# Kernel tuning notes

Measured on AMD Instinct MI355X. Metric: run time of the kernel, lower is better.

## Reference

```python
import jax, jax.numpy as jnp
import numpy as np

EPS = 1e-08   # clip eps from __init__
M = 0.2       # angular margin
B, D, C = 512, 512, 100000


def setup_inputs() -> dict:
    key = jax.random.key(0)
    k1, k2, k3 = jax.random.split(key, 3)
    x = jax.random.normal(k1, (B, D), dtype=jnp.float32)
    weight = jax.random.normal(k2, (C, D), dtype=jnp.float32)
    y = jax.random.randint(k3, (B,), 0, C, dtype=jnp.int64)
    rescale = jnp.ones((1,), dtype=jnp.float32)
    return {"x": x, "y": y, "weight": weight, "rescale": rescale}


def _l2norm(v, axis=-1, eps=1e-12):
    # matches F.normalize(p=2): v / max(||v||, eps)
    n = jnp.sqrt(jnp.sum(v * v, axis=axis, keepdims=True))
    return v / jnp.maximum(n, eps)


def reference(x, y, weight, rescale):
    # cos similarities: [B, C]
    fc = jnp.clip(_l2norm(x) @ _l2norm(weight).T, -1.0 + EPS, 1.0 - EPS)
    fc_w_margin = jnp.cos(jnp.arccos(fc) + M)
    # inject margin only at the target class (one-hot where-select)
    is_target = jax.nn.one_hot(y, C, dtype=jnp.bool_)
    logit = jnp.where(is_target, fc_w_margin, fc)
    # faithful to original: softmax, then CrossEntropyLoss on the probs
    res = jax.nn.softmax(rescale * logit, axis=-1)
    logp = jax.nn.log_softmax(res, axis=-1)
    nll = -jnp.take_along_axis(logp, y[:, None], axis=1)[:, 0]
    return jnp.mean(nll)
```

## Files before the change

kernel.cpp:

```cpp
#include <hip/hip_runtime.h>
#include <math.h>

#define BB 512
#define DD 512
#define CC 100000
#define CCPAD 100096
#define MARGIN 0.2f
#define CLIP_EPS 1e-8f
#define NCOLT 782

typedef float f32x4  __attribute__((ext_vector_type(4)));
typedef long  lx2    __attribute__((ext_vector_type(2)));

#define XN8_BYTES   262144u
#define P_BYTES     1601536u
#define PBASE       XN8_BYTES
#define AUX_OFF     (PBASE + 3u * P_BYTES)

__device__ inline unsigned f2e4m3(float a) {
    unsigned u = __builtin_bit_cast(unsigned, a);
    unsigned s = (u >> 24) & 0x80u;
    float ab = fabsf(a);
    unsigned code;
    if (ab >= 0.015625f) {
        unsigned r = (u & 0x7FFFFFFFu) + 0x7FFFFu + ((u >> 20) & 1u);
        int e = (int)(r >> 23) - 127;
        unsigned m = (r >> 20) & 7u;
        code = (unsigned)((e + 7) << 3) | m;
    } else {
        code = (unsigned)rintf(ab * 512.0f);
    }
    return s | code;
}

__device__ inline int soff8(int row, int b) {
    return row * 64 + ((((b >> 4) ^ ((row >> 1) & 3)) << 4)) + (b & 15);
}


__global__ __launch_bounds__(256) void k_prep(const float* __restrict__ w,
                                              const float* __restrict__ x,
                                              unsigned char* __restrict__ WN8,
                                              unsigned char* __restrict__ XN8,
                                              float* __restrict__ out) {
    int wv = threadIdx.x >> 6, lane = threadIdx.x & 63;
    int r = blockIdx.x * 4 + wv;
    const float* src;
    unsigned char* dst;
    bool zero = false;
    if (r < CCPAD) {
        zero = (r >= CC);
        src = w + (size_t)(zero ? 0 : r) * DD;
        dst = WN8 + (size_t)r * DD;
    } else {
        int xr = r - CCPAD;
        src = x + (size_t)xr * DD;
        dst = XN8 + (size_t)xr * DD;
    }
    int o  = lane * 8;
    int K0 = (o & ~63) + ((o >> 3) & 1) * 32 + ((o >> 4) & 3) * 8;
    float4 a = *(const float4*)(src + K0);
    float4 b = *(const float4*)(src + K0 + 4);
    if (zero) { a = make_float4(0.f,0.f,0.f,0.f); b = a; }
    float ss = a.x*a.x + a.y*a.y + a.z*a.z + a.w*a.w
             + b.x*b.x + b.y*b.y + b.z*b.z + b.w*b.w;
    for (int m = 1; m < 64; m <<= 1) ss += __shfl_xor(ss, m, 64);
    float inv = 1.0f / fmaxf(sqrtf(ss), 1e-12f);
    unsigned lo = f2e4m3(a.x*inv) | (f2e4m3(a.y*inv) << 8) | (f2e4m3(a.z*inv) << 16) | (f2e4m3(a.w*inv) << 24);
    unsigned hi = f2e4m3(b.x*inv) | (f2e4m3(b.y*inv) << 8) | (f2e4m3(b.z*inv) << 16) | (f2e4m3(b.w*inv) << 24);
    *(uint2*)(dst + o) = make_uint2(lo, hi);
    if (blockIdx.x == 0 && threadIdx.x == 0) out[0] = 0.0f;
}

__global__ __launch_bounds__(256) void k_gemm8(const unsigned char* __restrict__ WN8,
                                               const unsigned char* __restrict__ XN8,
                                               const float* __restrict__ rescale_p,
                                               float* __restrict__ ZP,
                                               float* __restrict__ S2P,
                                               float* __restrict__ S3P) {
    __shared__ __align__(16) unsigned char Wt[3][128 * 64];
    __shared__ __align__(16) unsigned char Xs[3][128 * 64];
    __shared__ float st[2][2][64][3];

    int h = blockIdx.x;
    int logical = (h & 7) * 391 + (h >> 3);
    int ct = logical >> 2;
    int bt = logical & 3;

    int tid = threadIdx.x;
    int lane = tid & 63, wid = tid >> 6;
    int wr = wid >> 1, wc = wid & 1;
    float rescale = rescale_p[0];

    int rl0 = wid * 16 + (lane >> 2);
    int j0  = lane & 3;
    const unsigned char* wbase = WN8 + (size_t)(ct * 128) * DD;
    const unsigned char* xbase = XN8 + (size_t)(bt * 128) * DD;

    auto STAGE = [&](int b, int kt) {
#pragma unroll
        for (int i = 0; i < 2; ++i) {
            int rl = i * 64 + rl0;
            int jsrc = j0 ^ ((rl >> 1) & 3);
            const unsigned char* ws_ = wbase + (size_t)rl * DD + kt * 64 + jsrc * 16;
            const unsigned char* xs_ = xbase + (size_t)rl * DD + kt * 64 + jsrc * 16;
            unsigned char* wd = &Wt[b][(i * 256 + wid * 64) * 16];
            unsigned char* xd = &Xs[b][(i * 256 + wid * 64) * 16];
            __builtin_amdgcn_global_load_lds(
                (const __attribute__((address_space(1))) void*)ws_,
                (__attribute__((address_space(3))) void*)wd, 16, 0, 0);
            __builtin_amdgcn_global_load_lds(
                (const __attribute__((address_space(1))) void*)xs_,
                (__attribute__((address_space(3))) void*)xd, 16, 0, 0);
        }
    };

    int roA[4], roB[4];
#pragma unroll
    for (int i = 0; i < 4; ++i) {
        int kb = (lane >> 4) * 16;
        roA[i] = soff8(wr * 64 + i * 16 + (lane & 15), kb);
        roB[i] = soff8(wc * 64 + i * 16 + (lane & 15), kb);
    }

    f32x4 acc[4][4];
#pragma unroll
    for (int i = 0; i < 4; i++)
#pragma unroll
        for (int j = 0; j < 4; j++) acc[i][j] = (f32x4){0.f, 0.f, 0.f, 0.f};

    auto COMPUTE = [&](int b) {
        lx2 a[4], bb[4];
#pragma unroll
        for (int i = 0; i < 4; i++) a[i]  = *(const lx2*)&Wt[b][roA[i]];
#pragma unroll
        for (int i = 0; i < 4; i++) bb[i] = *(const lx2*)&Xs[b][roB[i]];
#pragma unroll
        for (int i = 0; i < 4; i++)
#pragma unroll
            for (int j = 0; j < 4; j++)
                acc[i][j] = __builtin_amdgcn_mfma_f32_16x16x32_fp8_fp8(a[i][0], bb[j][0], acc[i][j], 0, 0, 0);
#pragma unroll
        for (int i = 0; i < 4; i++)
#pragma unroll
            for (int j = 0; j < 4; j++)
                acc[i][j] = __builtin_amdgcn_mfma_f32_16x16x32_fp8_fp8(a[i][1], bb[j][1], acc[i][j], 0, 0, 0);
    };

    STAGE(0, 0);
    STAGE(1, 1);
    STAGE(2, 2);
    asm volatile("s_waitcnt vmcnt(8)" ::: "memory");
    __builtin_amdgcn_s_barrier();

    int cur = 0;
    for (int kt = 0; kt < 8; ++kt) {
        COMPUTE(cur);
        if (kt == 7) break;
        __builtin_amdgcn_s_barrier();
        if (kt < 5) {
            STAGE(cur, kt + 3);
            asm volatile("s_waitcnt vmcnt(8)" ::: "memory");
        } else if (kt == 5) {
            asm volatile("s_waitcnt vmcnt(4)" ::: "memory");
        } else {
            asm volatile("s_waitcnt vmcnt(0)" ::: "memory");
        }
        __builtin_amdgcn_s_barrier();
        cur = (cur == 2) ? 0 : cur + 1;
    }

    float mref = fabsf(rescale);
    const float L2E = 1.44269504f;
    float rs = rescale * L2E, mb = mref * L2E;
    float zz[4] = {0.f,0.f,0.f,0.f}, q2[4] = {0.f,0.f,0.f,0.f}, q3[4] = {0.f,0.f,0.f,0.f};
#pragma unroll
    for (int mi = 0; mi < 4; mi++) {
#pragma unroll
        for (int reg = 0; reg < 4; reg++) {
            int c = ct * 128 + wr * 64 + mi * 16 + (lane >> 4) * 4 + reg;
            float mask = (c < CC) ? 1.0f : 0.0f;
#pragma unroll
            for (int ni = 0; ni < 4; ni++) {
                float cosv = acc[mi][ni][reg];
                cosv = fminf(fmaxf(cosv, -1.0f + CLIP_EPS), 1.0f - CLIP_EPS);
                float e = exp2f(fmaf(cosv, rs, -mb)) * mask;
                float e2 = e * e;
                zz[ni] += e;
                q2[ni] += e2;
                q3[ni] = fmaf(e2, e, q3[ni]);
            }
        }
    }
#pragma unroll
    for (int msk = 16; msk < 64; msk <<= 1) {
#pragma unroll
        for (int ni = 0; ni < 4; ni++) {
            zz[ni] += __shfl_xor(zz[ni], msk, 64);
            q2[ni] += __shfl_xor(q2[ni], msk, 64);
            q3[ni] += __shfl_xor(q3[ni], msk, 64);
        }
    }
    if (lane < 16) {
#pragma unroll
        for (int ni = 0; ni < 4; ni++) {
            st[wc][wr][ni * 16 + lane][0] = zz[ni];
            st[wc][wr][ni * 16 + lane][1] = q2[ni];
            st[wc][wr][ni * 16 + lane][2] = q3[ni];
        }
    }
    __syncthreads();
    if (tid < 128) {
        int bh = tid >> 6, bl = tid & 63;
        float Z  = st[bh][0][bl][0] + st[bh][1][bl][0];
        float S2 = st[bh][0][bl][1] + st[bh][1][bl][1];
        float S3 = st[bh][0][bl][2] + st[bh][1][bl][2];
        size_t gi = (size_t)ct * BB + bt * 128 + tid;
        ZP[gi] = Z; S2P[gi] = S2; S3P[gi] = S3;
    }
}

__global__ __launch_bounds__(256) void k_final(const float* __restrict__ x,
                                               const float* __restrict__ w,
                                               const int* __restrict__ y,
                                               const float* __restrict__ rescale_p,
                                               const float* __restrict__ ZP,
                                               const float* __restrict__ S2P,
                                               const float* __restrict__ S3P,
                                               float* __restrict__ out) {
    int b = blockIdx.x, tid = threadIdx.x;
    int yb = y[b];

    float dq = 0.f, qx = 0.f, qw = 0.f;
#pragma unroll
    for (int i = 0; i < 2; i++) {
        int idx = tid + i * 256;
        float xv = x[b * DD + idx];
        float wv = w[(size_t)yb * DD + idx];
        dq = fmaf(xv, wv, dq);
        qx = fmaf(xv, xv, qx);
        qw = fmaf(wv, wv, qw);
    }
    for (int m = 1; m < 64; m <<= 1) {
        dq += __shfl_xor(dq, m, 64);
        qx += __shfl_xor(qx, m, 64);
        qw += __shfl_xor(qw, m, 64);
    }
    __shared__ float sd[4], sx[4], sw[4], szs[4], s2s[4], s3s[4];
    int wid = tid >> 6, lane = tid & 63;
    if (lane == 0) { sd[wid] = dq; sx[wid] = qx; sw[wid] = qw; }

    float rz = 0.f, r2 = 0.f, r3 = 0.f;
    for (int ch = tid; ch < NCOLT; ch += 256) {
        size_t gi = (size_t)ch * BB + b;
        rz += ZP[gi]; r2 += S2P[gi]; r3 += S3P[gi];
    }
    for (int m = 1; m < 64; m <<= 1) {
        rz += __shfl_xor(rz, m, 64);
        r2 += __shfl_xor(r2, m, 64);
        r3 += __shfl_xor(r3, m, 64);
    }
    if (lane == 0) { szs[wid] = rz; s2s[wid] = r2; s3s[wid] = r3; }
    __syncthreads();

    if (tid == 0) {
        float Z  = szs[0] + szs[1] + szs[2] + szs[3];
        float S2 = s2s[0] + s2s[1] + s2s[2] + s2s[3];
        float S3 = s3s[0] + s3s[1] + s3s[2] + s3s[3];
        float dot = sd[0] + sd[1] + sd[2] + sd[3];
        float ssx = sx[0] + sx[1] + sx[2] + sx[3];
        float ssw = sw[0] + sw[1] + sw[2] + sw[3];
        float rescale = rescale_p[0];
        float mref = fabsf(rescale);
        float fc = dot / (fmaxf(sqrtf(ssx), 1e-12f) * fmaxf(sqrtf(ssw), 1e-12f));
        fc = fminf(fmaxf(fc, -1.0f + CLIP_EPS), 1.0f - CLIP_EPS);
        float su = rescale * fc;
        float fcm = fc * cosf(MARGIN) - sqrtf(fmaxf(1.0f - fc * fc, 0.0f)) * sinf(MARGIN);
        float smv = rescale * fcm;
        float eU = __expf(su - mref), eM = __expf(smv - mref);
        Z  += eM - eU;
        S2 += eM * eM - eU * eU;
        S3 += eM * eM * eM - eU * eU * eU;
        float py = eM / Z;
        float sumexp = (float)CC + 1.0f + S2 / (2.0f * Z * Z) + S3 / (6.0f * Z * Z * Z);
        float nll = logf(sumexp) - py;
        atomicAdd(out, nll * (1.0f / (float)BB));
    }
}

extern "C" void kernel_launch(void* const* d_in, const int* in_sizes, int n_in,
                              void* d_out, int out_size, void* d_ws, size_t ws_size,
                              hipStream_t stream) {
    const float* x       = (const float*)d_in[0];
    const int*   y       = (const int*)  d_in[1];
    const float* w       = (const float*)d_in[2];
    const float* rescale = (const float*)d_in[3];
    float* out = (float*)d_out;
    char*  wsb = (char*)d_ws;

    unsigned char* XN8 = (unsigned char*)(wsb);
    float* ZP  = (float*)(wsb + PBASE);
    float* S2P = (float*)(wsb + PBASE + P_BYTES);
    float* S3P = (float*)(wsb + PBASE + 2u * P_BYTES);
    unsigned char* WN8 = (unsigned char*)(wsb + AUX_OFF);

    k_prep  <<<dim3(CCPAD / 4 + BB / 4), dim3(256), 0, stream>>>(w, x, WN8, XN8, out);
    k_gemm8 <<<dim3(8 * 391), dim3(256), 0, stream>>>(WN8, XN8, rescale, ZP, S2P, S3P);
    k_final <<<dim3(BB), dim3(256), 0, stream>>>(x, w, y, rescale, ZP, S2P, S3P, out);
}
```

Measured before the change: 105.6 us.

## Fuse weight normalization and fp8 quantization into the GEMM kernel

Drops the separate pass over the weight matrix that wrote a normalized fp8 copy to workspace. The GEMM kernel now loads fp32 weight rows into registers, converts them to fp8 into a double-buffered LDS tile and accumulates their squared norms on the fly. The inverse norm is applied to the accumulators in the epilogue instead. This removes a full write and re-read of the quantized weights, but each weight tile is now read in fp32 and converted once per batch tile. It also quantizes unnormalized weights, which slightly changes rounding behaviour.

```diff
diff --git a/kernel.cpp b/kernel.cpp
--- a/kernel.cpp
+++ b/kernel.cpp
@@ -4,7 +4,6 @@
 #define BB 512
 #define DD 512
 #define CC 100000
-#define CCPAD 100096
 #define MARGIN 0.2f
 #define CLIP_EPS 1e-8f
 #define NCOLT 782
@@ -15,7 +14,6 @@
 #define XN8_BYTES   262144u
 #define P_BYTES     1601536u
 #define PBASE       XN8_BYTES
-#define AUX_OFF     (PBASE + 3u * P_BYTES)
 
 __device__ inline unsigned f2e4m3(float a) {
     unsigned u = __builtin_bit_cast(unsigned, a);
@@ -38,30 +36,17 @@
 }
 
 
-__global__ __launch_bounds__(256) void k_prep(const float* __restrict__ w,
-                                              const float* __restrict__ x,
-                                              unsigned char* __restrict__ WN8,
+__global__ __launch_bounds__(256) void k_prep(const float* __restrict__ x,
                                               unsigned char* __restrict__ XN8,
                                               float* __restrict__ out) {
     int wv = threadIdx.x >> 6, lane = threadIdx.x & 63;
     int r = blockIdx.x * 4 + wv;
-    const float* src;
-    unsigned char* dst;
-    bool zero = false;
-    if (r < CCPAD) {
-        zero = (r >= CC);
-        src = w + (size_t)(zero ? 0 : r) * DD;
-        dst = WN8 + (size_t)r * DD;
-    } else {
-        int xr = r - CCPAD;
-        src = x + (size_t)xr * DD;
-        dst = XN8 + (size_t)xr * DD;
-    }
+    const float* src = x + (size_t)r * DD;
+    unsigned char* dst = XN8 + (size_t)r * DD;
     int o  = lane * 8;
     int K0 = (o & ~63) + ((o >> 3) & 1) * 32 + ((o >> 4) & 3) * 8;
     float4 a = *(const float4*)(src + K0);
     float4 b = *(const float4*)(src + K0 + 4);
-    if (zero) { a = make_float4(0.f,0.f,0.f,0.f); b = a; }
     float ss = a.x*a.x + a.y*a.y + a.z*a.z + a.w*a.w
              + b.x*b.x + b.y*b.y + b.z*b.z + b.w*b.w;
     for (int m = 1; m < 64; m <<= 1) ss += __shfl_xor(ss, m, 64);
@@ -72,15 +57,16 @@
     if (blockIdx.x == 0 && threadIdx.x == 0) out[0] = 0.0f;
 }
 
-__global__ __launch_bounds__(256) void k_gemm8(const unsigned char* __restrict__ WN8,
+__global__ __launch_bounds__(256) void k_gemmf(const float* __restrict__ w,
                                                const unsigned char* __restrict__ XN8,
                                                const float* __restrict__ rescale_p,
                                                float* __restrict__ ZP,
                                                float* __restrict__ S2P,
                                                float* __restrict__ S3P) {
-    __shared__ __align__(16) unsigned char Wt[3][128 * 64];
     __shared__ __align__(16) unsigned char Xs[3][128 * 64];
+    __shared__ __align__(16) unsigned char Wt[2][128 * 64];
     __shared__ float st[2][2][64][3];
+    __shared__ float wsum[128];
 
     int h = blockIdx.x;
     int logical = (h & 7) * 391 + (h >> 3);
@@ -94,24 +80,40 @@
 
     int rl0 = wid * 16 + (lane >> 2);
     int j0  = lane & 3;
-    const unsigned char* wbase = WN8 + (size_t)(ct * 128) * DD;
     const unsigned char* xbase = XN8 + (size_t)(bt * 128) * DD;
-
-    auto STAGE = [&](int b, int kt) {
+    auto STAGE_X = [&](int b, int kt) {
 #pragma unroll
         for (int i = 0; i < 2; ++i) {
             int rl = i * 64 + rl0;
             int jsrc = j0 ^ ((rl >> 1) & 3);
-            const unsigned char* ws_ = wbase + (size_t)rl * DD + kt * 64 + jsrc * 16;
             const unsigned char* xs_ = xbase + (size_t)rl * DD + kt * 64 + jsrc * 16;
-            unsigned char* wd = &Wt[b][(i * 256 + wid * 64) * 16];
             unsigned char* xd = &Xs[b][(i * 256 + wid * 64) * 16];
-            __builtin_amdgcn_global_load_lds(
-                (const __attribute__((address_space(1))) void*)ws_,
-                (__attribute__((address_space(3))) void*)wd, 16, 0, 0);
             __builtin_amdgcn_global_load_lds(
                 (const __attribute__((address_space(1))) void*)xs_,
                 (__attribute__((address_space(3))) void*)xd, 16, 0, 0);
+        }
+    };
+
+    int wrl = tid >> 1, kh = tid & 1;
+    int cg = ct * 128 + wrl;
+    int cgc = cg < CC ? cg : CC - 1;
+    const float4* wsrc = (const float4*)(w + (size_t)cgc * DD + kh * 32);
+
+    float4 wrg[2][8];
+    float swacc = 0.f;
+    auto WLOAD = [&](int slot, int kt) {
+#pragma unroll
+        for (int q = 0; q < 8; ++q) wrg[slot][q] = wsrc[kt * 16 + q];
+    };
+    auto CONV_W = [&](int slot, int buf) {
+#pragma unroll
+        for (int q = 0; q < 4; ++q) {
+            float4 a = wrg[slot][2 * q], b = wrg[slot][2 * q + 1];
+            swacc += a.x*a.x + a.y*a.y + a.z*a.z + a.w*a.w
+                   + b.x*b.x + b.y*b.y + b.z*b.z + b.w*b.w;
+            unsigned lo = f2e4m3(a.x) | (f2e4m3(a.y) << 8) | (f2e4m3(a.z) << 16) | (f2e4m3(a.w) << 24);
+            unsigned hi = f2e4m3(b.x) | (f2e4m3(b.y) << 8) | (f2e4m3(b.z) << 16) | (f2e4m3(b.w) << 24);
+            *(uint2*)&Wt[buf][soff8(wrl, 16 * q + 8 * kh)] = make_uint2(lo, hi);
         }
     };
 
@@ -129,12 +131,12 @@
 #pragma unroll
         for (int j = 0; j < 4; j++) acc[i][j] = (f32x4){0.f, 0.f, 0.f, 0.f};
 
-    auto COMPUTE = [&](int b) {
+    auto COMPUTE = [&](int xb, int wb) {
         lx2 a[4], bb[4];
 #pragma unroll
-        for (int i = 0; i < 4; i++) a[i]  = *(const lx2*)&Wt[b][roA[i]];
-#pragma unroll
-        for (int i = 0; i < 4; i++) bb[i] = *(const lx2*)&Xs[b][roB[i]];
+        for (int i = 0; i < 4; i++) a[i]  = *(const lx2*)&Wt[wb][roA[i]];
+#pragma unroll
+        for (int i = 0; i < 4; i++) bb[i] = *(const lx2*)&Xs[xb][roB[i]];
 #pragma unroll
         for (int i = 0; i < 4; i++)
 #pragma unroll
@@ -147,28 +149,32 @@
                 acc[i][j] = __builtin_amdgcn_mfma_f32_16x16x32_fp8_fp8(a[i][1], bb[j][1], acc[i][j], 0, 0, 0);
     };
 
-    STAGE(0, 0);
-    STAGE(1, 1);
-    STAGE(2, 2);
+    STAGE_X(0, 0); STAGE_X(1, 1); STAGE_X(2, 2);
+    WLOAD(0, 0); WLOAD(1, 1);
     asm volatile("s_waitcnt vmcnt(8)" ::: "memory");
+    CONV_W(0, 0);
+    asm volatile("s_waitcnt lgkmcnt(0)" ::: "memory");
     __builtin_amdgcn_s_barrier();
 
-    int cur = 0;
+#pragma unroll
     for (int kt = 0; kt < 8; ++kt) {
-        COMPUTE(cur);
+        COMPUTE(kt % 3, kt & 1);
         if (kt == 7) break;
         __builtin_amdgcn_s_barrier();
-        if (kt < 5) {
-            STAGE(cur, kt + 3);
-            asm volatile("s_waitcnt vmcnt(8)" ::: "memory");
-        } else if (kt == 5) {
-            asm volatile("s_waitcnt vmcnt(4)" ::: "memory");
-        } else {
-            asm volatile("s_waitcnt vmcnt(0)" ::: "memory");
-        }
+        if (kt + 3 <= 7) STAGE_X(kt % 3, kt + 3);
+        if (kt + 2 <= 7) WLOAD(kt & 1, kt + 2);
+        if (kt <= 4)      { asm volatile("s_waitcnt vmcnt(10)" ::: "memory"); }
+        else if (kt == 5) { asm volatile("s_waitcnt vmcnt(8)" ::: "memory"); }
+        else              { asm volatile("s_waitcnt vmcnt(0)" ::: "memory"); }
+        CONV_W((kt + 1) & 1, (kt + 1) & 1);
+        asm volatile("s_waitcnt lgkmcnt(0)" ::: "memory");
         __builtin_amdgcn_s_barrier();
-        cur = (cur == 2) ? 0 : cur + 1;
-    }
+    }
+
+    swacc += __shfl_xor(swacc, 1, 64);
+    __syncthreads();
+    if (kh == 0) wsum[wrl] = swacc;
+    __syncthreads();
 
     float mref = fabsf(rescale);
     const float L2E = 1.44269504f;
@@ -178,11 +184,13 @@
     for (int mi = 0; mi < 4; mi++) {
 #pragma unroll
         for (int reg = 0; reg < 4; reg++) {
-            int c = ct * 128 + wr * 64 + mi * 16 + (lane >> 4) * 4 + reg;
+            int cl = wr * 64 + mi * 16 + (lane >> 4) * 4 + reg;
+            int c  = ct * 128 + cl;
             float mask = (c < CC) ? 1.0f : 0.0f;
+            float winv = 1.0f / fmaxf(sqrtf(wsum[cl]), 1e-12f);
 #pragma unroll
             for (int ni = 0; ni < 4; ni++) {
-                float cosv = acc[mi][ni][reg];
+                float cosv = acc[mi][ni][reg] * winv;
                 cosv = fminf(fmaxf(cosv, -1.0f + CLIP_EPS), 1.0f - CLIP_EPS);
                 float e = exp2f(fmaf(cosv, rs, -mb)) * mask;
                 float e2 = e * e;
@@ -302,9 +310,8 @@
     float* ZP  = (float*)(wsb + PBASE);
     float* S2P = (float*)(wsb + PBASE + P_BYTES);
     float* S3P = (float*)(wsb + PBASE + 2u * P_BYTES);
-    unsigned char* WN8 = (unsigned char*)(wsb + AUX_OFF);
-
-    k_prep  <<<dim3(CCPAD / 4 + BB / 4), dim3(256), 0, stream>>>(w, x, WN8, XN8, out);
-    k_gemm8 <<<dim3(8 * 391), dim3(256), 0, stream>>>(WN8, XN8, rescale, ZP, S2P, S3P);
+
+    k_prep  <<<dim3(BB / 4), dim3(256), 0, stream>>>(x, XN8, out);
+    k_gemmf <<<dim3(8 * 391), dim3(256), 0, stream>>>(w, XN8, rescale, ZP, S2P, S3P);
     k_final <<<dim3(BB), dim3(256), 0, stream>>>(x, w, y, rescale, ZP, S2P, S3P, out);
 }
```

New measurement: 317.0 us. 3x slower.

## Hold X fragments in registers and stream only W through a 4-stage LDS ring

Applied to the files above, without the earlier changes.

The GEMM kernel now loads each wave's full X operand (all 8 k-tiles) directly from global memory into registers at the start, so only the W tile is staged through LDS. The W stage uses a 4-buffer ring indexed by kt, which removes one of the two barriers per k-step. The loop is fully unrolled with sched_barriers and two blocks per CU are requested. The aim is to halve LDS traffic and synchronisation per step, at the cost of many more VGPRs (64 lx2 values), which may cause spills under the 2-block occupancy bound.

```diff
diff --git a/kernel.cpp b/kernel.cpp
--- a/kernel.cpp
+++ b/kernel.cpp
@@ -72,14 +72,13 @@
     if (blockIdx.x == 0 && threadIdx.x == 0) out[0] = 0.0f;
 }
 
-__global__ __launch_bounds__(256) void k_gemm8(const unsigned char* __restrict__ WN8,
-                                               const unsigned char* __restrict__ XN8,
-                                               const float* __restrict__ rescale_p,
-                                               float* __restrict__ ZP,
-                                               float* __restrict__ S2P,
-                                               float* __restrict__ S3P) {
-    __shared__ __align__(16) unsigned char Wt[3][128 * 64];
-    __shared__ __align__(16) unsigned char Xs[3][128 * 64];
+__global__ __launch_bounds__(256, 2) void k_gemmx(const unsigned char* __restrict__ WN8,
+                                                  const unsigned char* __restrict__ XN8,
+                                                  const float* __restrict__ rescale_p,
+                                                  float* __restrict__ ZP,
+                                                  float* __restrict__ S2P,
+                                                  float* __restrict__ S3P) {
+    __shared__ __align__(16) unsigned char Wt[4][128 * 64];
     __shared__ float st[2][2][64][3];
 
     int h = blockIdx.x;
@@ -95,32 +94,35 @@
     int rl0 = wid * 16 + (lane >> 2);
     int j0  = lane & 3;
     const unsigned char* wbase = WN8 + (size_t)(ct * 128) * DD;
-    const unsigned char* xbase = XN8 + (size_t)(bt * 128) * DD;
-
-    auto STAGE = [&](int b, int kt) {
+    auto STAGE_W = [&](int b, int kt) {
 #pragma unroll
         for (int i = 0; i < 2; ++i) {
             int rl = i * 64 + rl0;
             int jsrc = j0 ^ ((rl >> 1) & 3);
             const unsigned char* ws_ = wbase + (size_t)rl * DD + kt * 64 + jsrc * 16;
-            const unsigned char* xs_ = xbase + (size_t)rl * DD + kt * 64 + jsrc * 16;
             unsigned char* wd = &Wt[b][(i * 256 + wid * 64) * 16];
-            unsigned char* xd = &Xs[b][(i * 256 + wid * 64) * 16];
             __builtin_amdgcn_global_load_lds(
                 (const __attribute__((address_space(1))) void*)ws_,
                 (__attribute__((address_space(3))) void*)wd, 16, 0, 0);
-            __builtin_amdgcn_global_load_lds(
-                (const __attribute__((address_space(1))) void*)xs_,
-                (__attribute__((address_space(3))) void*)xd, 16, 0, 0);
         }
     };
 
-    int roA[4], roB[4];
-#pragma unroll
-    for (int i = 0; i < 4; ++i) {
-        int kb = (lane >> 4) * 16;
-        roA[i] = soff8(wr * 64 + i * 16 + (lane & 15), kb);
-        roB[i] = soff8(wc * 64 + i * 16 + (lane & 15), kb);
+    int roA[4];
+#pragma unroll
+    for (int i = 0; i < 4; ++i)
+        roA[i] = soff8(wr * 64 + i * 16 + (lane & 15), (lane >> 4) * 16);
+
+    lx2 xf[8][4];
+    {
+        const unsigned char* xb = XN8 + (size_t)(bt * 128 + wc * 64 + (lane & 15)) * DD
+                                + (lane >> 4) * 16;
+#pragma unroll
+        for (int ni = 0; ni < 4; ++ni) {
+            const unsigned char* xr = xb + (size_t)(ni * 16) * DD;
+#pragma unroll
+            for (int kt = 0; kt < 8; ++kt)
+                xf[kt][ni] = *(const lx2*)(xr + kt * 64);
+        }
     }
 
     f32x4 acc[4][4];
@@ -129,45 +131,37 @@
 #pragma unroll
         for (int j = 0; j < 4; j++) acc[i][j] = (f32x4){0.f, 0.f, 0.f, 0.f};
 
-    auto COMPUTE = [&](int b) {
-        lx2 a[4], bb[4];
-#pragma unroll
-        for (int i = 0; i < 4; i++) a[i]  = *(const lx2*)&Wt[b][roA[i]];
-#pragma unroll
-        for (int i = 0; i < 4; i++) bb[i] = *(const lx2*)&Xs[b][roB[i]];
-#pragma unroll
-        for (int i = 0; i < 4; i++)
-#pragma unroll
-            for (int j = 0; j < 4; j++)
-                acc[i][j] = __builtin_amdgcn_mfma_f32_16x16x32_fp8_fp8(a[i][0], bb[j][0], acc[i][j], 0, 0, 0);
-#pragma unroll
-        for (int i = 0; i < 4; i++)
-#pragma unroll
-            for (int j = 0; j < 4; j++)
-                acc[i][j] = __builtin_amdgcn_mfma_f32_16x16x32_fp8_fp8(a[i][1], bb[j][1], acc[i][j], 0, 0, 0);
-    };
-
-    STAGE(0, 0);
-    STAGE(1, 1);
-    STAGE(2, 2);
-    asm volatile("s_waitcnt vmcnt(8)" ::: "memory");
+    STAGE_W(0, 0);
+    STAGE_W(1, 1);
+    STAGE_W(2, 2);
+    asm volatile("s_waitcnt vmcnt(4)" ::: "memory");
+    __builtin_amdgcn_sched_barrier(0);
     __builtin_amdgcn_s_barrier();
 
-    int cur = 0;
+#pragma unroll
     for (int kt = 0; kt < 8; ++kt) {
-        COMPUTE(cur);
+        {
+            lx2 a[4];
+#pragma unroll
+            for (int i = 0; i < 4; i++) a[i] = *(const lx2*)&Wt[kt & 3][roA[i]];
+#pragma unroll
+            for (int i = 0; i < 4; i++)
+#pragma unroll
+                for (int j = 0; j < 4; j++)
+                    acc[i][j] = __builtin_amdgcn_mfma_f32_16x16x32_fp8_fp8(a[i][0], xf[kt][j][0], acc[i][j], 0, 0, 0);
+#pragma unroll
+            for (int i = 0; i < 4; i++)
+#pragma unroll
+                for (int j = 0; j < 4; j++)
+                    acc[i][j] = __builtin_amdgcn_mfma_f32_16x16x32_fp8_fp8(a[i][1], xf[kt][j][1], acc[i][j], 0, 0, 0);
+        }
         if (kt == 7) break;
+        if (kt + 3 <= 7) STAGE_W((kt + 3) & 3, kt + 3);
+        if (kt <= 4)      { asm volatile("s_waitcnt vmcnt(4)" ::: "memory"); }
+        else if (kt == 5) { asm volatile("s_waitcnt vmcnt(2)" ::: "memory"); }
+        else              { asm volatile("s_waitcnt vmcnt(0)" ::: "memory"); }
+        __builtin_amdgcn_sched_barrier(0);
         __builtin_amdgcn_s_barrier();
-        if (kt < 5) {
-            STAGE(cur, kt + 3);
-            asm volatile("s_waitcnt vmcnt(8)" ::: "memory");
-        } else if (kt == 5) {
-            asm volatile("s_waitcnt vmcnt(4)" ::: "memory");
-        } else {
-            asm volatile("s_waitcnt vmcnt(0)" ::: "memory");
-        }
-        __builtin_amdgcn_s_barrier();
-        cur = (cur == 2) ? 0 : cur + 1;
     }
 
     float mref = fabsf(rescale);
@@ -305,6 +299,6 @@
     unsigned char* WN8 = (unsigned char*)(wsb + AUX_OFF);
 
     k_prep  <<<dim3(CCPAD / 4 + BB / 4), dim3(256), 0, stream>>>(w, x, WN8, XN8, out);
-    k_gemm8 <<<dim3(8 * 391), dim3(256), 0, stream>>>(WN8, XN8, rescale, ZP, S2P, S3P);
+    k_gemmx <<<dim3(8 * 391), dim3(256), 0, stream>>>(WN8, XN8, rescale, ZP, S2P, S3P);
     k_final <<<dim3(BB), dim3(256), 0, stream>>>(x, w, y, rescale, ZP, S2P, S3P, out);
 }
```

Result: slower. 138.8 us (+31.5%).
